# Kernel optimization log

Measured on AMD Instinct MI355X. Metric: run time of the kernel, lower is better.

## Reference

```python
import jax, jax.numpy as jnp
from jax import lax
import numpy as np

DN = ('NCHW', 'OIHW', 'NCHW')

def _conv(x, w, b, s):
    # torch Conv2d(kernel=3, padding=1, stride=s)
    y = lax.conv_general_dilated(x, w, (s, s), ((1, 1), (1, 1)), dimension_numbers=DN)
    return y + b[None, :, None, None]

def _convT(x, w, b, s):
    # torch ConvTranspose2d weight layout [in, out, kh, kw]; kernel=3, padding=1, output_padding=s-1
    wk = jnp.flip(w, (2, 3)).transpose(1, 0, 2, 3)  # -> OIHW
    y = lax.conv_general_dilated(x, wk, (1, 1), ((1, s), (1, s)), lhs_dilation=(s, s), dimension_numbers=DN)
    return y + b[None, :, None, None]

def _inorm(x, eps=1e-5):
    # torch InstanceNorm2d (affine=False)
    m = jnp.mean(x, (2, 3), keepdims=True)
    v = jnp.var(x, (2, 3), keepdims=True)
    return (x - m) * lax.rsqrt(v + eps)

def _prelu(x, a):
    return jnp.where(x >= 0, x, a * x)

def _block(x, w, b, a, s):
    return _prelu(_inorm(_conv(x, w, b, s)), a)

def _sage(x, src, tgt, wl, bl, wr, n):
    # PyG SAGEConv, mean aggregation: lin_l(scatter_mean(x[src] -> tgt)) + lin_r(x)
    deg = jnp.zeros((n,), x.dtype).at[tgt].add(1.0)
    agg = jnp.zeros((x.shape[0], n, x.shape[2]), x.dtype).at[:, tgt].add(x[:, src])
    agg = agg / jnp.maximum(deg, 1.0)[None, :, None]
    return jnp.einsum('bnc,oc->bno', agg, wl) + bl + jnp.einsum('bnc,oc->bno', x, wr)

def setup_inputs() -> dict:
    keys = iter(jax.random.split(jax.random.key(0), 64))
    def rn(shape, s=0.05):
        return jax.random.normal(next(keys), shape, jnp.float32) * s
    inp = {}
    inp['x'] = jax.random.normal(next(keys), (16, 1, 400, 400), jnp.float32)
    inp['edges'] = jax.random.randint(next(keys), (2, 5000), 0, 625, jnp.int32)
    for name, (ci, co) in zip(['d4', 'd3', 'd2', 'd1'], [(1, 32), (32, 64), (64, 128), (128, 256)]):
        inp['w_' + name] = rn((co, ci, 3, 3)); inp['b_' + name] = rn((co,))
        inp['a_' + name] = jnp.full((1,), 0.25, jnp.float32)
    inp['w_bot'] = rn((256, 256, 3, 3)); inp['b_bot'] = rn((256,))
    inp['a_bot'] = jnp.full((1,), 0.25, jnp.float32)
    for i in ['1', '2']:
        inp['wl' + i] = rn((256, 256)); inp['bl' + i] = rn((256,)); inp['wr' + i] = rn((256, 256))
    for name, (ci, co) in zip(['u1', 'u2', 'u3'], [(512, 128), (256, 64), (128, 32)]):
        inp['w_' + name] = rn((ci, co, 3, 3)); inp['b_' + name] = rn((co,))
        inp['a_' + name] = jnp.full((1,), 0.25, jnp.float32)
    inp['w_u4'] = rn((64, 2, 3, 3)); inp['b_u4'] = rn((2,))
    return inp

def reference(x, edges, w_d4, b_d4, a_d4, w_d3, b_d3, a_d3, w_d2, b_d2, a_d2, w_d1, b_d1, a_d1, w_bot, b_bot, a_bot, wl1, bl1, wr1, wl2, bl2, wr2, w_u1, b_u1, a_u1, w_u2, b_u2, a_u2, w_u3, b_u3, a_u3, w_u4, b_u4):
    xs = []
    x = _block(x, w_d4, b_d4, a_d4, 2); xs.append(x)   # [B,32,200,200]
    x = _block(x, w_d3, b_d3, a_d3, 2); xs.append(x)   # [B,64,100,100]
    x = _block(x, w_d2, b_d2, a_d2, 2); xs.append(x)   # [B,128,50,50]
    x = _block(x, w_d1, b_d1, a_d1, 2); xs.append(x)   # [B,256,25,25]
    x = _block(x, w_bot, b_bot, a_bot, 1)              # [B,256,25,25]
    B = x.shape[0]
    x = x.reshape(B, 256, -1).transpose(0, 2, 1)       # [B,625,256]
    src, tgt = edges[0], edges[1]
    x = jax.nn.relu(_sage(x, src, tgt, wl1, bl1, wr1, 625))
    x = jax.nn.relu(_sage(x, src, tgt, wl2, bl2, wr2, 625))
    x = x.transpose(0, 2, 1).reshape(B, 256, 25, 25)
    x = jnp.concatenate([xs[3], x], 1)                 # 512 ch
    x = _prelu(_inorm(_convT(x, w_u1, b_u1, 2)), a_u1) # [B,128,50,50]
    x = jnp.concatenate([xs[2], x], 1)
    x = _prelu(_inorm(_convT(x, w_u2, b_u2, 2)), a_u2) # [B,64,100,100]
    x = jnp.concatenate([xs[1], x], 1)
    x = _prelu(_inorm(_convT(x, w_u3, b_u3, 2)), a_u3) # [B,32,200,200]
    x = jnp.concatenate([xs[0], x], 1)
    return _convT(x, w_u4, b_u4, 2)                    # [B,2,400,400], conv_only top
```

## Files before the change

kernel.cpp:

```cpp
#include <hip/hip_runtime.h>
#include <hip/hip_bf16.h>

typedef __hip_bfloat16 bf16;

typedef __bf16 bf16x8 __attribute__((ext_vector_type(8)));
typedef float  f32x16 __attribute__((ext_vector_type(16)));

static __device__ __forceinline__ float bf(const bf16 v){ return __bfloat162float(v); }
static __device__ __forceinline__ float bfu(unsigned short u){
  unsigned fw = ((unsigned)u) << 16; float v; __builtin_memcpy(&v, &fw, 4); return v;
}

static __device__ __forceinline__ float ldm(const void* p, long i, int f){
  return f ? ((const float*)p)[i] : __bfloat162float(((const bf16*)p)[i]);
}
static __device__ __forceinline__ void stm(void* p, long i, int f, float v){
  if(f) ((float*)p)[i] = v; else ((bf16*)p)[i] = __float2bfloat16(v);
}
static __device__ __forceinline__ unsigned short bfbits(float v){
  __hip_bfloat16 h = __float2bfloat16(v);
  return *(unsigned short*)&h;
}

__global__ void k_detect(const void* __restrict__ w, int* __restrict__ mode){
  if(blockIdx.x == 0 && threadIdx.x == 0){
    const unsigned int* u = (const unsigned int*)w;
    int saneLo = 0;
    for(int i = 0; i < 64; i++){
      unsigned short lo = (unsigned short)(u[i] & 0xFFFFu);
      unsigned int fw = ((unsigned int)lo) << 16;
      float v; __builtin_memcpy(&v, &fw, 4);
      float a = fabsf(v);
      if(a > 1e-7f && a < 100.f) saneLo++;
    }
    *mode = (saneLo >= 48) ? 0 : 1;
  }
}

__global__ void k_wtrans6(const void* __restrict__ w, bf16* __restrict__ wF,
                          const int* __restrict__ dmode){
  int idx = blockIdx.x * 256 + threadIdx.x;
  if(idx >= 65536) return;
  int dm = *dmode;
  int e = idx & 7;
  int L = (idx >> 3) & 63;
  int r = idx >> 9;
  int nc = r & 7;
  int kc = r >> 3;
  int o = nc*32 + (L & 31);
  int c = kc*16 + (L >> 5)*8 + e;
  wF[idx] = __float2bfloat16(ldm(w, (long)o*256 + c, dm));
}

__global__ void k_wtrans4(const void* __restrict__ w, bf16* __restrict__ wF,
                          const int* __restrict__ dmode, int Cin, int Cout){
  int idx = blockIdx.x * 256 + threadIdx.x;
  if(idx >= Cin * Cout * 9) return;
  int dm = *dmode;
  int e = idx & 7;
  int L = (idx >> 3) & 63;
  int r = idx >> 9;
  int NC = Cout >> 5;
  int nc = r % NC; r /= NC;
  int t  = r % 9;
  int kc = r / 9;
  int ci = kc*16 + (L>>5)*8 + e;
  int co = nc*32 + (L&31);
  wF[idx] = __float2bfloat16(ldm(w, ((long)ci*Cout + co)*9 + t, dm));
}

__global__ void k_wtrans5(const void* __restrict__ w, bf16* __restrict__ wF,
                          const int* __restrict__ dmode, int Cin, int Cout){
  int idx = blockIdx.x * 256 + threadIdx.x;
  if(idx >= Cin * Cout * 9) return;
  int dm = *dmode;
  int e = idx & 7;
  int L = (idx >> 3) & 63;
  int r = idx >> 9;
  int NC = Cout >> 5;
  int nc = r % NC; r /= NC;
  int t  = r % 9;
  int kc = r / 9;
  int ci = kc*16 + (L>>5)*8 + e;
  int co = nc*32 + (L&31);
  wF[idx] = __float2bfloat16(ldm(w, ((long)co*Cin + ci)*9 + t, dm));
}

__global__ __launch_bounds__(256, 4)
void k_conv_d4(const void* __restrict__ in, long in_off,
               const void* __restrict__ w, const void* __restrict__ bias,
               bf16* __restrict__ out, const int* __restrict__ dmode)
{
  __shared__ float sW[288];
  __shared__ float sB[32];
  int tid = threadIdx.x;
  int dm = *dmode;
  for(int e = tid; e < 288; e += 256) sW[e] = ldm(w, e, dm);
  if(tid < 32)  sB[tid] = ldm(bias, tid, dm);
  __syncthreads();
  int r = tid / 50, jt = tid % 50;
  if(r >= 5) return;
  int ho = blockIdx.x * 5 + r;
  int b  = blockIdx.z;
  int j0 = jt * 4;

  float x[3][9];
  long ibase = in_off + (long)b * 160000;
  #pragma unroll
  for(int rr = 0; rr < 3; rr++){
    int ir = 2*ho - 1 + rr;
    if(ir < 0 || ir >= 400){
      #pragma unroll
      for(int c = 0; c < 9; c++) x[rr][c] = 0.f;
      continue;
    }
    long rb = ibase + (long)ir * 400;
    int c0 = 2*j0 - 1;
    #pragma unroll
    for(int c = 0; c < 9; c++){
      int ic = c0 + c;
      x[rr][c] = (ic >= 0 && ic < 400) ? ldm(in, rb + ic, dm) : 0.f;
    }
  }

  long obase = ((long)b * 32) * 40000 + (long)ho * 200 + j0;
  for(int co = 0; co < 32; co++){
    const float* wv = &sW[co*9];
    float bv = sB[co];
    float a[4];
    #pragma unroll
    for(int p = 0; p < 4; p++){
      float s = bv;
      #pragma unroll
      for(int kh = 0; kh < 3; kh++)
        #pragma unroll
        for(int kw = 0; kw < 3; kw++)
          s += x[kh][2*p + kw] * wv[kh*3 + kw];
      a[p] = s;
    }
    ushort4 pk;
    pk.x = bfbits(a[0]); pk.y = bfbits(a[1]); pk.z = bfbits(a[2]); pk.w = bfbits(a[3]);
    *(ushort4*)&out[obase + (long)co * 40000] = pk;
  }
}

template<int CW, int NWC, int NWM, int S, int OCC>
__global__ __launch_bounds__(256, OCC)
void k_convSM(const void* __restrict__ in, long in_off, int fin_sel,
              const bf16* __restrict__ wF, const void* __restrict__ bias,
              void* __restrict__ out, int fout,
              const int* __restrict__ dmode,
              int Cin, int Hin, int Win, int Cout, int Hout, int Wout, int nym)
{
  constexpr int CP = 40;
  constexpr int HALF = CW/2;
  __shared__ unsigned short sX[3*CW*CP];
  int tid  = threadIdx.x;
  int lane = tid & 63;
  int wv   = tid >> 6;
  int nc   = wv % NWC;
  int mt   = wv / NWC;
  int ho   = blockIdx.x;
  int colg = blockIdx.y % nym;
  int cog  = blockIdx.y / nym;
  int b    = blockIdx.z;
  int dm   = *dmode;
  int fin  = (fin_sel == 2) ? dm : fin_sel;
  int NCtot = Cout >> 5;
  int chunk = cog*NWC + nc;
  int jl   = mt*32 + (lane & 31);
  int hi   = lane >> 5;
  int C0   = S*(colg*NWM*32);
  int ir0  = S*ho - 1;

  f32x16 acc;
  #pragma unroll
  for(int q = 0; q < 16; q++) acc[q] = 0.f;

  int p0, p1, p2;
  if(S == 2){ p0 = jl; p1 = HALF + jl; p2 = jl + 1; }
  else      { p0 = jl; p1 = jl + 1;    p2 = jl + 2; }

  for(int ci0 = 0; ci0 < Cin; ci0 += 32){
    for(int e = tid; e < 12*CW; e += 256){
      int c  = e % CW;
      int s  = e / CW;
      int kg = s & 3, r = s >> 2;
      int ir = ir0 + r;
      int ic = C0 - 1 + c;
      unsigned pk0, pk1, pk2, pk3;
      if(ir >= 0 && ir < Hin && ic >= 0 && ic < Win){
        long step = (long)Hin*Win;
        long base = in_off + ((long)b*Cin + ci0 + kg*8)*step + (long)ir*Win + ic;
        unsigned short t8[8];
        #pragma unroll
        for(int u = 0; u < 8; u++) t8[u] = bfbits(ldm(in, base + u*step, fin));
        pk0 = t8[0] | ((unsigned)t8[1]<<16);
        pk1 = t8[2] | ((unsigned)t8[3]<<16);
        pk2 = t8[4] | ((unsigned)t8[5]<<16);
        pk3 = t8[6] | ((unsigned)t8[7]<<16);
      } else { pk0=0; pk1=0; pk2=0; pk3=0; }
      int pos = (S == 2) ? ((c&1) ? HALF + (c>>1) : (c>>1)) : c;
      uint4 q; q.x=pk0; q.y=pk1; q.z=pk2; q.w=pk3;
      *(uint4*)&sX[(r*CW + pos)*CP + kg*8] = q;
    }
    __syncthreads();

    #pragma unroll
    for(int kg2 = 0; kg2 < 2; kg2++){
      int kbase = 8*hi + kg2*16;
      bf16x8 x[9];
      #pragma unroll
      for(int r = 0; r < 3; r++){
        x[r*3+0] = *(const bf16x8*)&sX[(r*CW + p0)*CP + kbase];
        x[r*3+1] = *(const bf16x8*)&sX[(r*CW + p1)*CP + kbase];
        x[r*3+2] = *(const bf16x8*)&sX[(r*CW + p2)*CP + kbase];
      }
      int kc = (ci0 >> 4) + kg2;
      const bf16x8* wb = ((const bf16x8*)wF) + ((long)(kc*9)*NCtot + chunk)*64 + lane;
      const long ws = (long)NCtot*64;
      #pragma unroll
      for(int t = 0; t < 9; t++){
        bf16x8 w = wb[(long)t*ws];
        acc = __builtin_amdgcn_mfma_f32_32x32x16_bf16(w, x[t], acc, 0,0,0);
      }
    }
    __syncthreads();
  }

  int j = colg*NWM*32 + jl;
  if(j < Wout){
    #pragma unroll
    for(int r16 = 0; r16 < 16; r16++){
      int co = chunk*32 + (r16&3) + 8*(r16>>2) + 4*hi;
      float bv = ldm(bias, co, dm);
      stm(out, ((long)b*Cout + co)*Hout*Wout + (long)ho*Wout + j, fout, acc[r16] + bv);
    }
  }
}

__global__ void k_inorm_prelu(void* __restrict__ x, int f, int HW,
                              const void* __restrict__ a, const int* __restrict__ dmode)
{
  int dm = *dmode;
  long base = (long)blockIdx.x * HW;
  float s = 0.f, s2 = 0.f;
  int vec = (f == 0) && ((HW & 3) == 0);
  if(vec){
    const ushort4* vp = (const ushort4*)((const bf16*)x + base);
    int n = HW >> 2;
    for(int i = threadIdx.x; i < n; i += 256){
      ushort4 v = vp[i];
      float a0 = bfu(v.x), a1 = bfu(v.y), a2 = bfu(v.z), a3 = bfu(v.w);
      s  += (a0 + a1) + (a2 + a3);
      s2 += (a0*a0 + a1*a1) + (a2*a2 + a3*a3);
    }
  } else {
    for(int i = threadIdx.x; i < HW; i += 256){ float v = ldm(x, base + i, f); s += v; s2 += v*v; }
  }
  __shared__ float sh[256], sh2[256];
  sh[threadIdx.x] = s; sh2[threadIdx.x] = s2; __syncthreads();
  for(int off = 128; off > 0; off >>= 1){
    if(threadIdx.x < off){ sh[threadIdx.x] += sh[threadIdx.x+off]; sh2[threadIdx.x] += sh2[threadIdx.x+off]; }
    __syncthreads();
  }
  float mean = sh[0] / HW;
  float var  = sh2[0] / HW - mean * mean;
  float inv  = rsqrtf(fmaxf(var, 0.f) + 1e-5f);
  float alpha = ldm(a, 0, dm);
  if(vec){
    ushort4* vp = (ushort4*)((bf16*)x + base);
    int n = HW >> 2;
    for(int i = threadIdx.x; i < n; i += 256){
      ushort4 v = vp[i];
      float t[4] = { bfu(v.x), bfu(v.y), bfu(v.z), bfu(v.w) };
      #pragma unroll
      for(int k = 0; k < 4; k++){
        float u = (t[k] - mean) * inv;
        t[k] = u >= 0.f ? u : alpha * u;
      }
      ushort4 o;
      o.x = bfbits(t[0]); o.y = bfbits(t[1]); o.z = bfbits(t[2]); o.w = bfbits(t[3]);
      vp[i] = o;
    }
  } else {
    for(int i = threadIdx.x; i < HW; i += 256){
      float v = (ldm(x, base + i, f) - mean) * inv;
      stm(x, base + i, f, v >= 0.f ? v : alpha * v);
    }
  }
}

__global__ void k_transpose(const float* __restrict__ in, float* __restrict__ out, int B, int C, int N){
  long idx = (long)blockIdx.x * 256 + threadIdx.x;
  long total = (long)B * C * N; if(idx >= total) return;
  int c = (int)(idx % C); long t = idx / C; int n = (int)(t % N); int b = (int)(t / N);
  out[idx] = in[((long)b * C + c) * N + n];
}

__global__ void k_deg(const int* __restrict__ tgt, float* __restrict__ deg, int E){
  int e = blockIdx.x * 256 + threadIdx.x;
  if(e < E) atomicAdd(&deg[tgt[e]], 1.0f);
}

__global__ void k_scatter(const float* __restrict__ xT, const int* __restrict__ src,
                          const int* __restrict__ tgt, float* __restrict__ agg,
                          int E, int C, int N, int B)
{
  int t = blockIdx.x * 256 + threadIdx.x;
  if(t >= E * C) return;
  int c = t % C; int e = t / C;
  int s = src[e], d = tgt[e];
  for(int b = 0; b < B; b++){
    atomicAdd(&agg[((long)b * N + d) * C + c], xT[((long)b * N + s) * C + c]);
  }
}

__global__ __launch_bounds__(256, 4)
void k_sageM(const float* __restrict__ xT, const float* __restrict__ agg,
             const float* __restrict__ deg,
             const bf16* __restrict__ wlF, const bf16* __restrict__ wrF,
             const void* __restrict__ bl,
             float* __restrict__ out, const int* __restrict__ dmode,
             int NROW, int trans)
{
  constexpr int CP = 264;
  __shared__ unsigned short sS[2*32*CP];
  int tid  = threadIdx.x;
  int lane = tid & 63;
  int wv   = tid >> 6;
  int ln   = lane & 31;
  int hi   = lane >> 5;
  int n0   = blockIdx.x * 32;
  int og0  = blockIdx.y * 128;
  int ncg  = blockIdx.y*4 + wv;
  int dm   = *dmode;

  for(int e = tid; e < 4096; e += 256){
    int c4 = e & 63;
    int r  = (e >> 6) & 31;
    int ar = e >> 11;
    int row = n0 + r;
    unsigned pk0 = 0, pk1 = 0;
    if(row < NROW){
      const float* sp = ar ? agg : xT;
      float4 v = *(const float4*)&sp[(long)row*256 + c4*4];
      if(ar){
        int n = row % 625;
        float dinv = 1.0f / fmaxf(deg[n], 1.0f);
        v.x *= dinv; v.y *= dinv; v.z *= dinv; v.w *= dinv;
      }
      pk0 = bfbits(v.x) | ((unsigned)bfbits(v.y) << 16);
      pk1 = bfbits(v.z) | ((unsigned)bfbits(v.w) << 16);
    }
    uint2 q; q.x = pk0; q.y = pk1;
    *(uint2*)&sS[(ar*32 + r)*CP + c4*4] = q;
  }
  __syncthreads();

  f32x16 acc;
  #pragma unroll
  for(int q = 0; q < 16; q++) acc[q] = 0.f;

  int xb = ln*CP + 8*hi;
  #pragma unroll
  for(int kc = 0; kc < 16; kc++){
    bf16x8 bx = *(const bf16x8*)&sS[xb + kc*16];
    bf16x8 ba = *(const bf16x8*)&sS[32*CP + xb + kc*16];
    bf16x8 wl = ((const bf16x8*)wlF)[(long)(kc*8 + ncg)*64 + lane];
    bf16x8 wr = ((const bf16x8*)wrF)[(long)(kc*8 + ncg)*64 + lane];
    acc = __builtin_amdgcn_mfma_f32_32x32x16_bf16(wl, ba, acc, 0,0,0);
    acc = __builtin_amdgcn_mfma_f32_32x32x16_bf16(wr, bx, acc, 0,0,0);
  }

  if(trans){
    int row = n0 + ln;
    if(row < NROW){
      int b = row / 625, n = row - b*625;
      #pragma unroll
      for(int r16 = 0; r16 < 16; r16++){
        int o = ncg*32 + (r16&3) + 8*(r16>>2) + 4*hi;
        float v = acc[r16] + ldm(bl, o, dm);
        out[((long)b*256 + o)*625 + n] = fmaxf(v, 0.f);
      }
    }
  } else {
    float* sO = (float*)sS;
    __syncthreads();
    #pragma unroll
    for(int r16 = 0; r16 < 16; r16++){
      int ol = wv*32 + (r16&3) + 8*(r16>>2) + 4*hi;
      float v = acc[r16] + ldm(bl, og0 + ol, dm);
      sO[ln*130 + ol] = fmaxf(v, 0.f);
    }
    __syncthreads();
    for(int e = tid; e < 4096; e += 256){
      int r = e >> 7, oc = e & 127;
      int row = n0 + r;
      if(row < NROW) out[(long)row*256 + og0 + oc] = sO[r*130 + oc];
    }
  }
}

template<int CW, int NWC, int NWM, int OCC>
__global__ __launch_bounds__(256, OCC)
void k_convTM(const void* __restrict__ inA, int fA, int C1,
              const void* __restrict__ inB, int fB, int C2,
              const bf16* __restrict__ wF, const void* __restrict__ bias,
              bf16* __restrict__ out, const int* __restrict__ dmode,
              int Hin, int Win, int Cout)
{
  constexpr int CP = 40;
  __shared__ unsigned short sX[2*CW*CP];
  int tid  = threadIdx.x;
  int lane = tid & 63;
  int wv   = tid >> 6;
  int nc   = wv % NWC;
  int mt   = wv / NWC;
  int j0   = mt * 32;
  int i    = blockIdx.x;
  int b    = blockIdx.z;
  int dm   = *dmode;
  int Cin  = C1 + C2;
  int ln   = lane & 31;
  int hi   = lane >> 5;

  f32x16 acc0, acc1, acc2, acc3;
  #pragma unroll
  for(int q = 0; q < 16; q++){ acc0[q]=0.f; acc1[q]=0.f; acc2[q]=0.f; acc3[q]=0.f; }

  int xoff = (j0 + ln)*CP + 8*hi;

  for(int ci0 = 0; ci0 < Cin; ci0 += 32){
    for(int e = tid; e < 8*CW; e += 256){
      int col = e % CW;
      int s   = e / CW;
      int kg  = s & 3, row = s >> 2;
      int ii  = i + row;
      unsigned pk0, pk1, pk2, pk3;
      if(ii < Hin && col < Win){
        int cib = ci0 + kg*8;
        const void* sp; int ff; long base; long step = (long)Hin*Win;
        if(cib < C1){ sp = inA; ff = fA; base = ((long)b*C1 + cib)*step + (long)ii*Win + col; }
        else        { sp = inB; ff = fB; base = ((long)b*C2 + (cib-C1))*step + (long)ii*Win + col; }
        unsigned short t8[8];
        #pragma unroll
        for(int u = 0; u < 8; u++) t8[u] = bfbits(ldm(sp, base + u*step, ff));
        pk0 = t8[0] | ((unsigned)t8[1]<<16);
        pk1 = t8[2] | ((unsigned)t8[3]<<16);
        pk2 = t8[4] | ((unsigned)t8[5]<<16);
        pk3 = t8[6] | ((unsigned)t8[7]<<16);
      } else { pk0=0; pk1=0; pk2=0; pk3=0; }
      uint4 q; q.x=pk0; q.y=pk1; q.z=pk2; q.w=pk3;
      *(uint4*)&sX[(row*CW + col)*CP + kg*8] = q;
    }
    __syncthreads();

    #pragma unroll
    for(int kg2 = 0; kg2 < 2; kg2++){
      int base = xoff + kg2*16;
      bf16x8 x00 = *(const bf16x8*)&sX[base];
      bf16x8 x01 = *(const bf16x8*)&sX[base + CP];
      bf16x8 x10 = *(const bf16x8*)&sX[base + CW*CP];
      bf16x8 x11 = *(const bf16x8*)&sX[base + CW*CP + CP];
      int kc = (ci0 >> 4) + kg2;
      const bf16x8* wb = ((const bf16x8*)wF) + ((long)(kc*9)*NWC + nc)*64 + lane;
      const int ws = NWC*64;
      bf16x8 w0=wb[0],    w1=wb[ws],   w2=wb[2*ws], w3=wb[3*ws], w4=wb[4*ws],
             w5=wb[5*ws], w6=wb[6*ws], w7=wb[7*ws], w8=wb[8*ws];
      acc0 = __builtin_amdgcn_mfma_f32_32x32x16_bf16(w4, x00, acc0, 0,0,0);
      acc1 = __builtin_amdgcn_mfma_f32_32x32x16_bf16(w5, x00, acc1, 0,0,0);
      acc1 = __builtin_amdgcn_mfma_f32_32x32x16_bf16(w3, x01, acc1, 0,0,0);
      acc2 = __builtin_amdgcn_mfma_f32_32x32x16_bf16(w7, x00, acc2, 0,0,0);
      acc2 = __builtin_amdgcn_mfma_f32_32x32x16_bf16(w1, x10, acc2, 0,0,0);
      acc3 = __builtin_amdgcn_mfma_f32_32x32x16_bf16(w8, x00, acc3, 0,0,0);
      acc3 = __builtin_amdgcn_mfma_f32_32x32x16_bf16(w6, x01, acc3, 0,0,0);
      acc3 = __builtin_amdgcn_mfma_f32_32x32x16_bf16(w2, x10, acc3, 0,0,0);
      acc3 = __builtin_amdgcn_mfma_f32_32x32x16_bf16(w0, x11, acc3, 0,0,0);
    }
    __syncthreads();
  }

  int j = j0 + ln;
  if(j < Win){
    int Wout = 2*Win;
    #pragma unroll
    for(int r = 0; r < 16; r++){
      int co = nc*32 + (r&3) + 8*(r>>2) + 4*hi;
      float bv = ldm(bias, co, dm);
      long base0 = (((long)b*Cout + co)*2*Hin + 2*i)*(long)Wout + 2*j;
      unsigned p0 = bfbits(acc0[r]+bv) | ((unsigned)bfbits(acc1[r]+bv) << 16);
      unsigned p1 = bfbits(acc2[r]+bv) | ((unsigned)bfbits(acc3[r]+bv) << 16);
      *(unsigned*)&out[base0]        = p0;
      *(unsigned*)&out[base0 + Wout] = p1;
    }
  }
}

__global__ __launch_bounds__(256, 2)
void k_convT8(const bf16* __restrict__ inA, const bf16* __restrict__ inB,
              const void* __restrict__ w, const void* __restrict__ bias,
              void* __restrict__ out, long out_off, int fout_sel,
              const int* __restrict__ dmode, int Hin, int Win)
{
  __shared__ float sW[64*2*9];
  __shared__ float sB[2];
  int tid = threadIdx.x;
  int dm = *dmode;
  for(int e = tid; e < 64*2*9; e += 256) sW[e] = ldm(w, e, dm);
  if(tid < 2) sB[tid] = ldm(bias, tid, dm);
  __syncthreads();
  int r  = tid / 50;
  int jt = tid % 50;
  if(r >= 5) return;
  int i  = blockIdx.x * 5 + r;
  int b  = blockIdx.z;
  int j0 = jt * 4;
  int fout = (fout_sel == 2) ? dm : fout_sel;

  float acc[2][4][4];
  #pragma unroll
  for(int co = 0; co < 2; co++)
    #pragma unroll
    for(int p = 0; p < 4; p++){
      acc[co][p][0]=0.f; acc[co][p][1]=0.f; acc[co][p][2]=0.f; acc[co][p][3]=0.f;
    }

  bool e4   = (j0 + 4 < Win);
  bool row1 = (i + 1 < Hin);

  for(int ci = 0; ci < 64; ci++){
    const bf16* src = (ci < 32) ? inA : inB;
    int cc = ci & 31;
    const bf16* rp = src + ((long)b*32 + cc)*(long)Hin*Win + (long)i*Win + j0;
    float x0[5], x1[5];
    ushort4 v0 = *(const ushort4*)rp;
    x0[0]=bfu(v0.x); x0[1]=bfu(v0.y); x0[2]=bfu(v0.z); x0[3]=bfu(v0.w);
    x0[4] = e4 ? bf(rp[4]) : 0.f;
    if(row1){
      ushort4 v1 = *(const ushort4*)(rp + Win);
      x1[0]=bfu(v1.x); x1[1]=bfu(v1.y); x1[2]=bfu(v1.z); x1[3]=bfu(v1.w);
      x1[4] = e4 ? bf(rp[Win + 4]) : 0.f;
    } else {
      x1[0]=0.f; x1[1]=0.f; x1[2]=0.f; x1[3]=0.f; x1[4]=0.f;
    }
    const float* wp = &sW[ci*18];
    float wv[18];
    #pragma unroll
    for(int k = 0; k < 18; k++) wv[k] = wp[k];
    #pragma unroll
    for(int p = 0; p < 4; p++){
      float a00 = x0[p], a01 = x0[p+1], a10 = x1[p], a11 = x1[p+1];
      #pragma unroll
      for(int co = 0; co < 2; co++){
        const float* wc = &wv[co*9];
        acc[co][p][0] += a00*wc[4];
        acc[co][p][1] += a00*wc[5] + a01*wc[3];
        acc[co][p][2] += a00*wc[7] + a10*wc[1];
        acc[co][p][3] += a00*wc[8] + a01*wc[6] + a10*wc[2] + a11*wc[0];
      }
    }
  }
  int Wout = 2*Win;
  #pragma unroll
  for(int co = 0; co < 2; co++){
    float bv = sB[co];
    long base = out_off + (((long)b*2 + co)*2*Hin + 2*i)*(long)Wout + 2*j0;
    #pragma unroll
    for(int p = 0; p < 4; p++){
      stm(out, base + 2*p,            fout, acc[co][p][0] + bv);
      stm(out, base + 2*p + 1,        fout, acc[co][p][1] + bv);
      stm(out, base + 2*p + Wout,     fout, acc[co][p][2] + bv);
      stm(out, base + 2*p + Wout + 1, fout, acc[co][p][3] + bv);
    }
  }
}

static inline int cdiv(long a, long b){ return (int)((a + b - 1) / b); }

extern "C" void kernel_launch(void* const* d_in, const int* in_sizes, int n_in,
                              void* d_out, int out_size, void* d_ws, size_t ws_size,
                              hipStream_t stream) {
  const void* x_in  = d_in[0];
  const int*  edges = (const int*)d_in[1];
  const int* src = edges;
  const int* tgt = edges + 5000;
  const void *w_d4=d_in[2],  *b_d4=d_in[3],  *a_d4=d_in[4];
  const void *w_d3=d_in[5],  *b_d3=d_in[6],  *a_d3=d_in[7];
  const void *w_d2=d_in[8],  *b_d2=d_in[9],  *a_d2=d_in[10];
  const void *w_d1=d_in[11], *b_d1=d_in[12], *a_d1=d_in[13];
  const void *w_bot=d_in[14],*b_bot=d_in[15],*a_bot=d_in[16];
  const void *wl1=d_in[17], *bl1=d_in[18], *wr1=d_in[19];
  const void *wl2=d_in[20], *bl2=d_in[21], *wr2=d_in[22];
  const void *w_u1=d_in[23], *b_u1=d_in[24], *a_u1=d_in[25];
  const void *w_u2=d_in[26], *b_u2=d_in[27], *a_u2=d_in[28];
  const void *w_u3=d_in[29], *b_u3=d_in[30], *a_u3=d_in[31];
  const void *w_u4=d_in[32], *b_u4=d_in[33];

  const int NNODE = 625, E = 5000, CG = 256;

  const long TAIL = 4096 + 4*262144L + (589824L + 147456L + 36864L) * 2;
  const long ENCW = 976896L * 2;
  int Bc = 16;
  while(Bc > 1 && (7680000L * Bc + TAIL) > (long)ws_size) Bc >>= 1;
  int enc_in_pool = (Bc >= 8);
  if(!enc_in_pool){
    Bc = 16;
    while(Bc > 1 && (7680000L * Bc + TAIL + ENCW) > (long)ws_size) Bc >>= 1;
  }

  char* wsb = (char*)d_ws;
  long o_xs1  = 2560000L * Bc;
  long o_BIGA = 3840000L * Bc;
  long o_BIGB = 6400000L * Bc;
  long o_deg  = 7680000L * Bc;
  bf16*  xs0 = (bf16*)wsb;
  bf16*  xs1 = (bf16*)(wsb + o_xs1);
  bf16*  xs2 = (bf16*)(wsb + o_BIGA);
  bf16*  xs3 = (bf16*)(wsb + o_BIGA +  640000L*Bc);
  float* bot = (float*)(wsb + o_BIGA +  960000L*Bc);
  float* xT  = (float*)(wsb + o_BIGA + 1600000L*Bc);
  bf16*  u1  = (bf16*)(wsb + o_BIGA + 1600000L*Bc);
  bf16*  u3  = (bf16*)(wsb + o_BIGA);
  float* agg = (float*)(wsb + o_BIGB);
  float* g1  = (float*)(wsb + o_BIGB +  640000L*Bc);
  bf16*  u2  = (bf16*)(wsb + o_BIGB);
  float* deg = (float*)(wsb + o_deg);
  int*  mode = (int*)(wsb + o_deg + 3072);
  bf16*  wlF1 = (bf16*)(wsb + o_deg + 4096);
  bf16*  wrF1 = wlF1 + 65536;
  bf16*  wlF2 = wrF1 + 65536;
  bf16*  wrF2 = wlF2 + 65536;
  bf16*  wTu1 = (bf16*)(wsb + o_deg + 4096 + 4*262144L);
  bf16*  wTu2 = wTu1 + 589824;
  bf16*  wTu3 = wTu2 + 147456;
  bf16*  wTd3 = enc_in_pool ? (bf16*)(wsb + o_BIGA + 2240000L*Bc) : (wTu3 + 36864);
  bf16*  wTd2 = wTd3 + 18432;
  bf16*  wTd1 = wTd2 + 73728;
  bf16*  wTdB = wTd1 + 294912;
  float* g2  = bot;

  hipLaunchKernelGGL(k_detect, dim3(1), dim3(1), 0, stream, w_d4, mode);

  hipMemsetAsync(deg, 0, NNODE*sizeof(float), stream);
  hipLaunchKernelGGL(k_deg, dim3(cdiv(E,256)), dim3(256), 0, stream, tgt, deg, E);
  hipLaunchKernelGGL(k_wtrans6, dim3(256), dim3(256), 0, stream, wl1, wlF1, mode);
  hipLaunchKernelGGL(k_wtrans6, dim3(256), dim3(256), 0, stream, wr1, wrF1, mode);
  hipLaunchKernelGGL(k_wtrans6, dim3(256), dim3(256), 0, stream, wl2, wlF2, mode);
  hipLaunchKernelGGL(k_wtrans6, dim3(256), dim3(256), 0, stream, wr2, wrF2, mode);
  hipLaunchKernelGGL(k_wtrans4, dim3(cdiv(589824,256)), dim3(256), 0, stream, w_u1, wTu1, mode, 512, 128);
  hipLaunchKernelGGL(k_wtrans4, dim3(cdiv(147456,256)), dim3(256), 0, stream, w_u2, wTu2, mode, 256, 64);
  hipLaunchKernelGGL(k_wtrans4, dim3(cdiv(36864,256)),  dim3(256), 0, stream, w_u3, wTu3, mode, 128, 32);

  for(int bo = 0; bo < 16; bo += Bc){
    long x_off   = (long)bo * 160000;
    long out_off = (long)bo * 320000;

    hipLaunchKernelGGL(k_wtrans5, dim3(cdiv(18432,256)),  dim3(256), 0, stream, w_d3, wTd3, mode, 32, 64);
    hipLaunchKernelGGL(k_wtrans5, dim3(cdiv(73728,256)),  dim3(256), 0, stream, w_d2, wTd2, mode, 64, 128);
    hipLaunchKernelGGL(k_wtrans5, dim3(cdiv(294912,256)), dim3(256), 0, stream, w_d1, wTd1, mode, 128, 256);
    hipLaunchKernelGGL(k_wtrans5, dim3(cdiv(589824,256)), dim3(256), 0, stream, w_bot, wTdB, mode, 256, 256);

    hipLaunchKernelGGL(k_conv_d4, dim3(40, 1, Bc), dim3(256), 0, stream,
                       x_in, x_off, w_d4, b_d4, xs0, mode);
    hipLaunchKernelGGL(k_inorm_prelu, dim3(Bc*32), dim3(256), 0, stream, xs0, 0, 40000, a_d4, mode);
    hipLaunchKernelGGL((k_convSM<130,2,2,2,4>), dim3(100, 2, Bc), dim3(256), 0, stream,
                       xs0, 0L, 0, wTd3, b_d3, xs1, 0, mode, 32, 200, 200, 64, 100, 100, 2);
    hipLaunchKernelGGL(k_inorm_prelu, dim3(Bc*64), dim3(256), 0, stream, xs1, 0, 10000, a_d3, mode);
    hipLaunchKernelGGL((k_convSM<66,4,1,2,4>), dim3(50, 2, Bc), dim3(256), 0, stream,
                       xs1, 0L, 0, wTd2, b_d2, xs2, 0, mode, 64, 100, 100, 128, 50, 50, 2);
    hipLaunchKernelGGL(k_inorm_prelu, dim3(Bc*128), dim3(256), 0, stream, xs2, 0, 2500, a_d2, mode);
    hipLaunchKernelGGL((k_convSM<66,4,1,2,4>), dim3(25, 2, Bc), dim3(256), 0, stream,
                       xs2, 0L, 0, wTd1, b_d1, xs3, 0, mode, 128, 50, 50, 256, 25, 25, 1);
    hipLaunchKernelGGL(k_inorm_prelu, dim3(Bc*256), dim3(256), 0, stream, xs3, 0, 625, a_d1, mode);
    hipLaunchKernelGGL((k_convSM<34,4,1,1,4>), dim3(25, 2, Bc), dim3(256), 0, stream,
                       xs3, 0L, 0, wTdB, b_bot, bot, 1, mode, 256, 25, 25, 256, 25, 25, 1);
    hipLaunchKernelGGL(k_inorm_prelu, dim3(Bc*256), dim3(256), 0, stream, bot, 1, 625, a_bot, mode);

    { long n = (long)Bc*CG*NNODE;
      hipLaunchKernelGGL(k_transpose, dim3(cdiv(n,256)), dim3(256), 0, stream, bot, xT, Bc, CG, NNODE); }
    hipMemsetAsync(agg, 0, 640000L*Bc, stream);
    hipLaunchKernelGGL(k_scatter, dim3(cdiv((long)E*CG,256)), dim3(256), 0, stream, xT, src, tgt, agg, E, CG, NNODE, Bc);
    hipLaunchKernelGGL(k_sageM, dim3(cdiv((long)Bc*NNODE,32), 2), dim3(256), 0, stream,
                       xT, agg, deg, wlF1, wrF1, bl1, g1, mode, Bc*NNODE, 0);
    hipMemsetAsync(agg, 0, 640000L*Bc, stream);
    hipLaunchKernelGGL(k_scatter, dim3(cdiv((long)E*CG,256)), dim3(256), 0, stream, g1, src, tgt, agg, E, CG, NNODE, Bc);
    hipLaunchKernelGGL(k_sageM, dim3(cdiv((long)Bc*NNODE,32), 2), dim3(256), 0, stream,
                       g1, agg, deg, wlF2, wrF2, bl2, g2, mode, Bc*NNODE, 1);

    hipLaunchKernelGGL((k_convTM<34,4,1,4>), dim3(25, 1, Bc), dim3(256), 0, stream,
                       xs3, 0, 256, g2, 1, 256, wTu1, b_u1, u1, mode, 25, 25, 128);
    hipLaunchKernelGGL(k_inorm_prelu, dim3(Bc*128), dim3(256), 0, stream, u1, 0, 2500, a_u1, mode);
    hipLaunchKernelGGL((k_convTM<66,2,2,4>), dim3(50, 1, Bc), dim3(256), 0, stream,
                       xs2, 0, 128, u1, 0, 128, wTu2, b_u2, u2, mode, 50, 50, 64);
    hipLaunchKernelGGL(k_inorm_prelu, dim3(Bc*64), dim3(256), 0, stream, u2, 0, 10000, a_u2, mode);
    hipLaunchKernelGGL((k_convTM<130,1,4,4>), dim3(100, 1, Bc), dim3(256), 0, stream,
                       xs1, 0, 64, u2, 0, 64, wTu3, b_u3, u3, mode, 100, 100, 32);
    hipLaunchKernelGGL(k_inorm_prelu, dim3(Bc*32), dim3(256), 0, stream, u3, 0, 40000, a_u3, mode);
    hipLaunchKernelGGL(k_convT8, dim3(40, 1, Bc), dim3(256), 0, stream,
                       xs0, u3, w_u4, b_u4, d_out, out_off, 2, mode, 200, 200);
  }
}
```

Measured before the change: 884.6 us.

## Stage each skip/upsampled channel half fully in LDS for transposed convs

The transposed-conv kernel now loads all channels of each input half (skip tensor, then decoder tensor) into LDS in one pass, instead of looping over 32-channel chunks. This cuts the number of barrier-separated load/compute phases to two per block and removes the per-chunk branch that chose between the two inputs. The LDS row pitch is padded per instantiation to limit bank conflicts. LDS per block grows to roughly 36 KB, which can reduce occupancy and removes the interleaving of small load and compute phases.

```diff
diff --git a/kernel.cpp b/kernel.cpp
--- a/kernel.cpp
+++ b/kernel.cpp
@@ -402,16 +402,15 @@
   }
 }
 
-template<int CW, int NWC, int NWM, int OCC>
+template<int CW, int NWC, int CC, int CIP, int OCC>
 __global__ __launch_bounds__(256, OCC)
-void k_convTM(const void* __restrict__ inA, int fA, int C1,
-              const void* __restrict__ inB, int fB, int C2,
+void k_convTF(const void* __restrict__ inA, int fA,
+              const void* __restrict__ inB, int fB,
               const bf16* __restrict__ wF, const void* __restrict__ bias,
               bf16* __restrict__ out, const int* __restrict__ dmode,
               int Hin, int Win, int Cout)
 {
-  constexpr int CP = 40;
-  __shared__ unsigned short sX[2*CW*CP];
+  __shared__ unsigned short sX[2*CW*CIP];
   int tid  = threadIdx.x;
   int lane = tid & 63;
   int wv   = tid >> 6;
@@ -421,28 +420,28 @@
   int i    = blockIdx.x;
   int b    = blockIdx.z;
   int dm   = *dmode;
-  int Cin  = C1 + C2;
   int ln   = lane & 31;
   int hi   = lane >> 5;
+  int NCtot = Cout >> 5;
 
   f32x16 acc0, acc1, acc2, acc3;
   #pragma unroll
   for(int q = 0; q < 16; q++){ acc0[q]=0.f; acc1[q]=0.f; acc2[q]=0.f; acc3[q]=0.f; }
 
-  int xoff = (j0 + ln)*CP + 8*hi;
-
-  for(int ci0 = 0; ci0 < Cin; ci0 += 32){
-    for(int e = tid; e < 8*CW; e += 256){
+  #pragma unroll
+  for(int half = 0; half < 2; half++){
+    const void* sp = half ? inB : inA;
+    int ff = half ? fB : fA;
+    for(int e = tid; e < 2*CW*(CC/8); e += 256){
       int col = e % CW;
       int s   = e / CW;
-      int kg  = s & 3, row = s >> 2;
+      int kg  = s % (CC/8);
+      int row = s / (CC/8);
       int ii  = i + row;
-      unsigned pk0, pk1, pk2, pk3;
+      unsigned pk0=0, pk1=0, pk2=0, pk3=0;
       if(ii < Hin && col < Win){
-        int cib = ci0 + kg*8;
-        const void* sp; int ff; long base; long step = (long)Hin*Win;
-        if(cib < C1){ sp = inA; ff = fA; base = ((long)b*C1 + cib)*step + (long)ii*Win + col; }
-        else        { sp = inB; ff = fB; base = ((long)b*C2 + (cib-C1))*step + (long)ii*Win + col; }
+        long step = (long)Hin*Win;
+        long base = ((long)b*CC + kg*8)*step + (long)ii*Win + col;
         unsigned short t8[8];
         #pragma unroll
         for(int u = 0; u < 8; u++) t8[u] = bfbits(ldm(sp, base + u*step, ff));
@@ -450,22 +449,21 @@
         pk1 = t8[2] | ((unsigned)t8[3]<<16);
         pk2 = t8[4] | ((unsigned)t8[5]<<16);
         pk3 = t8[6] | ((unsigned)t8[7]<<16);
-      } else { pk0=0; pk1=0; pk2=0; pk3=0; }
+      }
       uint4 q; q.x=pk0; q.y=pk1; q.z=pk2; q.w=pk3;
-      *(uint4*)&sX[(row*CW + col)*CP + kg*8] = q;
+      *(uint4*)&sX[(row*CW + col)*CIP + kg*8] = q;
     }
     __syncthreads();
 
-    #pragma unroll
-    for(int kg2 = 0; kg2 < 2; kg2++){
-      int base = xoff + kg2*16;
-      bf16x8 x00 = *(const bf16x8*)&sX[base];
-      bf16x8 x01 = *(const bf16x8*)&sX[base + CP];
-      bf16x8 x10 = *(const bf16x8*)&sX[base + CW*CP];
-      bf16x8 x11 = *(const bf16x8*)&sX[base + CW*CP + CP];
-      int kc = (ci0 >> 4) + kg2;
-      const bf16x8* wb = ((const bf16x8*)wF) + ((long)(kc*9)*NWC + nc)*64 + lane;
-      const int ws = NWC*64;
+    for(int kc = 0; kc < CC/16; kc++){
+      int kb = kc*16 + 8*hi;
+      bf16x8 x00 = *(const bf16x8*)&sX[(j0 + ln)*CIP + kb];
+      bf16x8 x01 = *(const bf16x8*)&sX[(j0 + ln + 1)*CIP + kb];
+      bf16x8 x10 = *(const bf16x8*)&sX[(CW + j0 + ln)*CIP + kb];
+      bf16x8 x11 = *(const bf16x8*)&sX[(CW + j0 + ln + 1)*CIP + kb];
+      int kcg = half*(CC/16) + kc;
+      const bf16x8* wb = ((const bf16x8*)wF) + ((long)(kcg*9)*NCtot + nc)*64 + lane;
+      const int ws = NCtot*64;
       bf16x8 w0=wb[0],    w1=wb[ws],   w2=wb[2*ws], w3=wb[3*ws], w4=wb[4*ws],
              w5=wb[5*ws], w6=wb[6*ws], w7=wb[7*ws], w8=wb[8*ws];
       acc0 = __builtin_amdgcn_mfma_f32_32x32x16_bf16(w4, x00, acc0, 0,0,0);
@@ -688,14 +686,14 @@
     hipLaunchKernelGGL(k_sageM, dim3(cdiv((long)Bc*NNODE,32), 2), dim3(256), 0, stream,
                        g1, agg, deg, wlF2, wrF2, bl2, g2, mode, Bc*NNODE, 1);
 
-    hipLaunchKernelGGL((k_convTM<34,4,1,4>), dim3(25, 1, Bc), dim3(256), 0, stream,
-                       xs3, 0, 256, g2, 1, 256, wTu1, b_u1, u1, mode, 25, 25, 128);
+    hipLaunchKernelGGL((k_convTF<34,4,256,264,4>), dim3(25, 1, Bc), dim3(256), 0, stream,
+                       xs3, 0, g2, 1, wTu1, b_u1, u1, mode, 25, 25, 128);
     hipLaunchKernelGGL(k_inorm_prelu, dim3(Bc*128), dim3(256), 0, stream, u1, 0, 2500, a_u1, mode);
-    hipLaunchKernelGGL((k_convTM<66,2,2,4>), dim3(50, 1, Bc), dim3(256), 0, stream,
-                       xs2, 0, 128, u1, 0, 128, wTu2, b_u2, u2, mode, 50, 50, 64);
+    hipLaunchKernelGGL((k_convTF<66,2,128,136,4>), dim3(50, 1, Bc), dim3(256), 0, stream,
+                       xs2, 0, u1, 0, wTu2, b_u2, u2, mode, 50, 50, 64);
     hipLaunchKernelGGL(k_inorm_prelu, dim3(Bc*64), dim3(256), 0, stream, u2, 0, 10000, a_u2, mode);
-    hipLaunchKernelGGL((k_convTM<130,1,4,4>), dim3(100, 1, Bc), dim3(256), 0, stream,
-                       xs1, 0, 64, u2, 0, 64, wTu3, b_u3, u3, mode, 100, 100, 32);
+    hipLaunchKernelGGL((k_convTF<130,1,64,72,4>), dim3(100, 1, Bc), dim3(256), 0, stream,
+                       xs1, 0, u2, 0, wTu3, b_u3, u3, mode, 100, 100, 32);
     hipLaunchKernelGGL(k_inorm_prelu, dim3(Bc*32), dim3(256), 0, stream, u3, 0, 40000, a_u3, mode);
     hipLaunchKernelGGL(k_convT8, dim3(40, 1, Bc), dim3(256), 0, stream,
                        xs0, u3, w_u4, b_u4, d_out, out_off, 2, mode, 200, 200);
```

After: 905.6 us. +2.4%, slower.
